# Kernel optimization log

Measured on AMD Instinct MI355X. Metric: run time of the kernel, lower is better.

The kernel has to match this reference:

```python
import jax, jax.numpy as jnp
import numpy as np

DT, TAU_S, TAU_M = 1.0, 4.0, 20.0
ALPHA = float(np.exp(-DT / TAU_S))   # synaptic current decay
BETA = float(np.exp(-DT / TAU_M))    # membrane potential decay
THRESH = 1.0
STEPS, BATCH, D1, D2 = 128, 256, 1024, 1024


def setup_inputs() -> dict:
    key = jax.random.key(0)
    k1, k2 = jax.random.split(key)
    inp = jax.random.uniform(k1, (STEPS, BATCH, D1), dtype=jnp.float32)
    # kaiming_normal_ on (d2, d1): std = sqrt(2 / fan_in), mu = 1.0
    weight = jax.random.normal(k2, (D2, D1), dtype=jnp.float32) * np.sqrt(2.0 / D1)
    return {"input": inp, "weight": weight}


def reference(input, weight):
    steps, batch = input.shape[0], input.shape[1]
    d2 = weight.shape[0]
    # Step i uses input[i-1]; precompute all linear projections at once.
    lin = jnp.einsum('tbi,oi->tbo', input[:-1], weight)  # [steps-1, B, d2]

    def step(carry, cur):
        syn, mem = carry
        # snntorch Synaptic, reset_mechanism='zero': reset from PREVIOUS mem
        reset = (mem > THRESH).astype(mem.dtype)
        syn = ALPHA * syn + cur
        mem = (BETA * mem + syn) * (1.0 - reset)
        spk = (mem > THRESH).astype(mem.dtype)
        return (syn, mem), (spk, mem, syn)

    init = (jnp.zeros((batch, d2), input.dtype), jnp.zeros((batch, d2), input.dtype))
    _, (spk, V, I) = jax.lax.scan(step, init, lin)
    z = jnp.zeros((1, batch, d2), input.dtype)  # step 0 stays zero
    output = jnp.concatenate([z, spk], axis=0)
    V = jnp.concatenate([z, V], axis=0)
    I = jnp.concatenate([z, I], axis=0)
    return output, V, I
```

## Files before the change

kernel.cpp:

```cpp
#include <hip/hip_runtime.h>
#include <hip/hip_fp16.h>


#define STEPS 128
#define BATCH 256
#define DIN   1024
#define DOUT  1024

#define ALPHA 0.7788007830714049f
#define BETA  0.9512294245007140f

constexpr int    GM      = (STEPS - 1) * BATCH;
constexpr size_t PLANE   = (size_t)BATCH * DOUT;
constexpr size_t A_ELEMS = (size_t)GM * DIN;
constexpr size_t W_ELEMS = (size_t)DOUT * DIN;

typedef __attribute__((ext_vector_type(8))) _Float16 half8;
typedef __attribute__((ext_vector_type(4))) float float4v;

__global__ __launch_bounds__(256)
void split_kernel(const float* __restrict__ x,
                  unsigned short* __restrict__ hi,
                  unsigned short* __restrict__ lo)
{
    const size_t i = (size_t)blockIdx.x * 256 + threadIdx.x;
    const float4 v = reinterpret_cast<const float4*>(x)[i];
    float f[4] = {v.x, v.y, v.z, v.w};
    unsigned short hb[4], lb[4];
#pragma unroll
    for (int j = 0; j < 4; ++j) {
        _Float16 h = (_Float16)f[j];
        _Float16 l = (_Float16)(f[j] - (float)h);
        hb[j] = *reinterpret_cast<unsigned short*>(&h);
        lb[j] = *reinterpret_cast<unsigned short*>(&l);
    }
    ushort4 hv = {hb[0], hb[1], hb[2], hb[3]};
    ushort4 lv = {lb[0], lb[1], lb[2], lb[3]};
    reinterpret_cast<ushort4*>(hi)[i] = hv;
    reinterpret_cast<ushort4*>(lo)[i] = lv;
}

__device__ __forceinline__ void load16(const unsigned short* g, unsigned short* l)
{
    __builtin_amdgcn_global_load_lds(
        (const __attribute__((address_space(1))) void*)g,
        (__attribute__((address_space(3))) void*)l, 16, 0, 0);
}

__device__ __forceinline__ half8 ldsr(unsigned addr)
{
    half8 r;
    asm volatile("ds_read_b128 %0, %1" : "=v"(r) : "v"(addr) : "memory");
    return r;
}

__global__ __launch_bounds__(512, 2)
void gemm_kernel(const unsigned short* __restrict__ Ah,
                 const unsigned short* __restrict__ Al,
                 const unsigned short* __restrict__ Wh,
                 const unsigned short* __restrict__ Wl,
                 float* __restrict__ C)
{
    __shared__ __align__(16) unsigned short smem[65536];

    const int lin = blockIdx.x;
    const int xcd = lin & 7, slot = lin >> 3;
    const int mp  = xcd * 16 + (slot >> 2);
    const int nt  = slot & 3;
    if (mp >= GM / 256) return;
    const int m0 = mp * 256;
    const int n0 = nt * 256;

    const int t = threadIdx.x;
    const int w = t >> 6, l = t & 63;
    const int wr = w >> 2, wc = w & 3;
    const int lr = l & 15, q = l >> 4;

    const int swz = q ^ ((l >> 1) & 3);

    const unsigned rdA = (unsigned)((wr * 128 + lr) * 64 + swz * 16);
    const unsigned rdB = (unsigned)(32768 + (wc * 64 + lr) * 64 + swz * 16);

    const int srow = l >> 2;
    const int sg   = ((l & 3) ^ ((l >> 3) & 3)) * 8;

    const size_t sA0 = (size_t)(m0 + w * 32 +      srow) * DIN + sg;
    const size_t sA1 = (size_t)(m0 + w * 32 + 16 + srow) * DIN + sg;
    const size_t sB0 = (size_t)(n0 + w * 32 +      srow) * DIN + sg;
    const size_t sB1 = (size_t)(n0 + w * 32 + 16 + srow) * DIN + sg;

    auto STAGE = [&](int ks) {
        const int kk = (ks & 31) << 5;
        unsigned short* d = smem + ((ks & 1) << 15) + w * 1024;
        load16(Ah + sA0 + kk, d);
        load16(Ah + sA1 + kk, d + 512);
        load16(Al + sA0 + kk, d + 8192);
        load16(Al + sA1 + kk, d + 8704);
        load16(Wh + sB0 + kk, d + 16384);
        load16(Wh + sB1 + kk, d + 16896);
        load16(Wl + sB0 + kk, d + 24576);
        load16(Wl + sB1 + kk, d + 25088);
    };

    float4v acc[8][4];
#pragma unroll
    for (int m = 0; m < 8; ++m)
#pragma unroll
        for (int n = 0; n < 4; ++n)
            acc[m][n] = (float4v){0.f, 0.f, 0.f, 0.f};

    STAGE(0);
    asm volatile("s_waitcnt vmcnt(0)" ::: "memory");
    __builtin_amdgcn_s_barrier();

    for (int kt = 0; kt < 32; ++kt) {
        const unsigned sb = (unsigned)((kt & 1) << 16);

        STAGE((kt + 1) & 31);

        half8 ah[8], bh[4], bl[4];

#pragma unroll
        for (int m = 0; m < 8; ++m) ah[m] = ldsr(sb + rdA + m * 1024);
#pragma unroll
        for (int n = 0; n < 4; ++n) bh[n] = ldsr(sb + rdB + n * 1024);
        asm volatile("s_waitcnt lgkmcnt(0)" ::: "memory");
        __builtin_amdgcn_sched_barrier(0);
        __builtin_amdgcn_s_setprio(1);
#pragma unroll
        for (int m = 0; m < 8; ++m)
#pragma unroll
            for (int n = 0; n < 4; ++n)
                acc[m][n] = __builtin_amdgcn_mfma_f32_16x16x32_f16(
                    ah[m], bh[n], acc[m][n], 0, 0, 0);
        __builtin_amdgcn_s_setprio(0);

#pragma unroll
        for (int n = 0; n < 4; ++n) bl[n] = ldsr(sb + rdB + 16384 + n * 1024);
        asm volatile("s_waitcnt lgkmcnt(0)" ::: "memory");
        __builtin_amdgcn_sched_barrier(0);
        __builtin_amdgcn_s_setprio(1);
#pragma unroll
        for (int m = 0; m < 8; ++m)
#pragma unroll
            for (int n = 0; n < 4; ++n)
                acc[m][n] = __builtin_amdgcn_mfma_f32_16x16x32_f16(
                    ah[m], bl[n], acc[m][n], 0, 0, 0);
        __builtin_amdgcn_s_setprio(0);

#pragma unroll
        for (int m = 0; m < 8; ++m) ah[m] = ldsr(sb + rdA + 16384 + m * 1024);
        asm volatile("s_waitcnt lgkmcnt(0)" ::: "memory");
        __builtin_amdgcn_sched_barrier(0);
        __builtin_amdgcn_s_setprio(1);
#pragma unroll
        for (int m = 0; m < 8; ++m)
#pragma unroll
            for (int n = 0; n < 4; ++n)
                acc[m][n] = __builtin_amdgcn_mfma_f32_16x16x32_f16(
                    ah[m], bh[n], acc[m][n], 0, 0, 0);
        __builtin_amdgcn_s_setprio(0);

        asm volatile("s_waitcnt vmcnt(0)" ::: "memory");
        __builtin_amdgcn_s_barrier();
    }

    const int mw = m0 + wr * 128 + q * 4;
    const int nw = n0 + wc * 64 + lr;
#pragma unroll
    for (int m = 0; m < 8; ++m)
#pragma unroll
        for (int n = 0; n < 4; ++n)
#pragma unroll
            for (int rg = 0; rg < 4; ++rg)
                C[(size_t)(mw + m * 16 + rg) * DOUT + (nw + n * 16)] = acc[m][n][rg];
}

__global__ __launch_bounds__(256)
void scan_kernel(float* __restrict__ out)
{
    const int idx = blockIdx.x * 256 + threadIdx.x;
    float* o0 = out;
    float* o1 = out + STEPS * PLANE;
    float* o2 = out + 2 * STEPS * PLANE;

    __builtin_nontemporal_store(0.0f, &o0[idx]);
    __builtin_nontemporal_store(0.0f, &o1[idx]);
    __builtin_nontemporal_store(0.0f, &o2[idx]);

    float n1 = o2[idx + PLANE];
    float n2 = o2[idx + 2 * PLANE];
    float n3 = o2[idx + 3 * PLANE];

    float syn = 0.0f, mem = 0.0f;
    size_t off = idx;
    for (int i = 1; i < STEPS; ++i) {
        off += PLANE;
        const float cur = n1; n1 = n2; n2 = n3;
        if (i + 3 < STEPS) n3 = o2[off + 3 * PLANE];
        const float reset = (mem > 1.0f) ? 1.0f : 0.0f;
        syn = ALPHA * syn + cur;
        mem = (BETA * mem + syn) * (1.0f - reset);
        const float spk = (mem > 1.0f) ? 1.0f : 0.0f;
        __builtin_nontemporal_store(spk, &o0[off]);
        __builtin_nontemporal_store(mem, &o1[off]);
        __builtin_nontemporal_store(syn, &o2[off]);
    }
}

extern "C" void kernel_launch(void* const* d_in, const int* in_sizes, int n_in,
                              void* d_out, int out_size, void* d_ws, size_t ws_size,
                              hipStream_t stream)
{
    const float* input  = (const float*)d_in[0];
    const float* weight = (const float*)d_in[1];
    float* out = (float*)d_out;

    unsigned short* Ah = (unsigned short*)out;
    unsigned short* Al = Ah + A_ELEMS;
    unsigned short* Wh = (unsigned short*)(out + STEPS * PLANE);
    unsigned short* Wl = Wh + W_ELEMS;
    float* lin = out + 2 * STEPS * PLANE + PLANE;

    split_kernel<<<(int)(A_ELEMS / 1024), 256, 0, stream>>>(input, Ah, Al);
    split_kernel<<<(int)(W_ELEMS / 1024), 256, 0, stream>>>(weight, Wh, Wl);

    gemm_kernel<<<512, 512, 0, stream>>>(Ah, Al, Wh, Wl, lin);

    scan_kernel<<<(int)(PLANE / 256), 256, 0, stream>>>(out);
}
```

Before: 686.5 us.

## Split GEMM k-loop into six barrier-synced phases with half-stage prefetch

The next k-tile's global-to-LDS staging is split into a hi half (A hi, W hi) and a lo half (A lo, W lo), each issued just before the phase that first needs it. A partial vmcnt(4) wait then lets the hi half of the next tile be consumed while the lo half is still in flight. Each of the three MFMA passes is split into two 4x4 sub-blocks, so only four A fragments are reloaded at a time, which lowers register pressure and interleaves LDS reads with matrix math. In exchange it adds many workgroup barriers per iteration, which may serialise the waves and hurt overlap between them.

```diff
diff --git a/kernel.cpp b/kernel.cpp
--- a/kernel.cpp
+++ b/kernel.cpp
@@ -54,6 +54,34 @@
     return r;
 }
 
+#define PHASE_PRE() do {                                        \
+    __builtin_amdgcn_s_barrier();                               \
+    asm volatile("s_waitcnt lgkmcnt(0)" ::: "memory");          \
+    __builtin_amdgcn_sched_barrier(0);                          \
+    __builtin_amdgcn_s_setprio(1);                              \
+} while (0)
+
+#define PHASE_POST() do {                                       \
+    __builtin_amdgcn_s_setprio(0);                              \
+    __builtin_amdgcn_sched_barrier(0);                          \
+    __builtin_amdgcn_s_barrier();                               \
+} while (0)
+
+#define PHASE_POST_VM4() do {                                   \
+    __builtin_amdgcn_s_setprio(0);                              \
+    __builtin_amdgcn_sched_barrier(0);                          \
+    asm volatile("s_waitcnt vmcnt(4)" ::: "memory");            \
+    __builtin_amdgcn_s_barrier();                               \
+} while (0)
+
+#define MFMA_BLK(MB, BV)                                        \
+    _Pragma("unroll")                                           \
+    for (int mm = 0; mm < 4; ++mm)                              \
+        _Pragma("unroll")                                       \
+        for (int nn = 0; nn < 4; ++nn)                          \
+            acc[(MB) + mm][nn] = __builtin_amdgcn_mfma_f32_16x16x32_f16( \
+                ah[(MB) + mm], BV[nn], acc[(MB) + mm][nn], 0, 0, 0)
+
 __global__ __launch_bounds__(512, 2)
 void gemm_kernel(const unsigned short* __restrict__ Ah,
                  const unsigned short* __restrict__ Al,
@@ -89,15 +117,19 @@
     const size_t sB0 = (size_t)(n0 + w * 32 +      srow) * DIN + sg;
     const size_t sB1 = (size_t)(n0 + w * 32 + 16 + srow) * DIN + sg;
 
-    auto STAGE = [&](int ks) {
+    auto STAGE_H1 = [&](int ks) {
         const int kk = (ks & 31) << 5;
         unsigned short* d = smem + ((ks & 1) << 15) + w * 1024;
         load16(Ah + sA0 + kk, d);
         load16(Ah + sA1 + kk, d + 512);
+        load16(Wh + sB0 + kk, d + 16384);
+        load16(Wh + sB1 + kk, d + 16896);
+    };
+    auto STAGE_H2 = [&](int ks) {
+        const int kk = (ks & 31) << 5;
+        unsigned short* d = smem + ((ks & 1) << 15) + w * 1024;
         load16(Al + sA0 + kk, d + 8192);
         load16(Al + sA1 + kk, d + 8704);
-        load16(Wh + sB0 + kk, d + 16384);
-        load16(Wh + sB1 + kk, d + 16896);
         load16(Wl + sB0 + kk, d + 24576);
         load16(Wl + sB1 + kk, d + 25088);
     };
@@ -109,60 +141,40 @@
         for (int n = 0; n < 4; ++n)
             acc[m][n] = (float4v){0.f, 0.f, 0.f, 0.f};
 
-    STAGE(0);
-    asm volatile("s_waitcnt vmcnt(0)" ::: "memory");
+    STAGE_H1(0);
+    STAGE_H2(0);
+    asm volatile("s_waitcnt vmcnt(4)" ::: "memory");
     __builtin_amdgcn_s_barrier();
 
     for (int kt = 0; kt < 32; ++kt) {
         const unsigned sb = (unsigned)((kt & 1) << 16);
-
-        STAGE((kt + 1) & 31);
-
         half8 ah[8], bh[4], bl[4];
 
 #pragma unroll
-        for (int m = 0; m < 8; ++m) ah[m] = ldsr(sb + rdA + m * 1024);
+        for (int m = 0; m < 4; ++m) ah[m] = ldsr(sb + rdA + m * 1024);
 #pragma unroll
         for (int n = 0; n < 4; ++n) bh[n] = ldsr(sb + rdB + n * 1024);
-        asm volatile("s_waitcnt lgkmcnt(0)" ::: "memory");
-        __builtin_amdgcn_sched_barrier(0);
-        __builtin_amdgcn_s_setprio(1);
-#pragma unroll
-        for (int m = 0; m < 8; ++m)
-#pragma unroll
-            for (int n = 0; n < 4; ++n)
-                acc[m][n] = __builtin_amdgcn_mfma_f32_16x16x32_f16(
-                    ah[m], bh[n], acc[m][n], 0, 0, 0);
-        __builtin_amdgcn_s_setprio(0);
+        STAGE_H1((kt + 1) & 31);
+        PHASE_PRE();  MFMA_BLK(0, bh);  PHASE_POST();
+
+#pragma unroll
+        for (int m = 4; m < 8; ++m) ah[m] = ldsr(sb + rdA + m * 1024);
+        PHASE_PRE();  MFMA_BLK(4, bh);  PHASE_POST_VM4();
 
 #pragma unroll
         for (int n = 0; n < 4; ++n) bl[n] = ldsr(sb + rdB + 16384 + n * 1024);
-        asm volatile("s_waitcnt lgkmcnt(0)" ::: "memory");
-        __builtin_amdgcn_sched_barrier(0);
-        __builtin_amdgcn_s_setprio(1);
-#pragma unroll
-        for (int m = 0; m < 8; ++m)
-#pragma unroll
-            for (int n = 0; n < 4; ++n)
-                acc[m][n] = __builtin_amdgcn_mfma_f32_16x16x32_f16(
-                    ah[m], bl[n], acc[m][n], 0, 0, 0);
-        __builtin_amdgcn_s_setprio(0);
-
-#pragma unroll
-        for (int m = 0; m < 8; ++m) ah[m] = ldsr(sb + rdA + 16384 + m * 1024);
-        asm volatile("s_waitcnt lgkmcnt(0)" ::: "memory");
-        __builtin_amdgcn_sched_barrier(0);
-        __builtin_amdgcn_s_setprio(1);
-#pragma unroll
-        for (int m = 0; m < 8; ++m)
-#pragma unroll
-            for (int n = 0; n < 4; ++n)
-                acc[m][n] = __builtin_amdgcn_mfma_f32_16x16x32_f16(
-                    ah[m], bh[n], acc[m][n], 0, 0, 0);
-        __builtin_amdgcn_s_setprio(0);
-
-        asm volatile("s_waitcnt vmcnt(0)" ::: "memory");
-        __builtin_amdgcn_s_barrier();
+        STAGE_H2((kt + 1) & 31);
+        PHASE_PRE();  MFMA_BLK(0, bl);  PHASE_POST();
+
+#pragma unroll
+        for (int m = 0; m < 4; ++m) ah[m] = ldsr(sb + rdA + 16384 + m * 1024);
+        PHASE_PRE();  MFMA_BLK(4, bl);  PHASE_POST();
+
+#pragma unroll
+        for (int m = 4; m < 8; ++m) ah[m] = ldsr(sb + rdA + 16384 + m * 1024);
+        PHASE_PRE();  MFMA_BLK(0, bh);  PHASE_POST();
+
+        PHASE_PRE();  MFMA_BLK(4, bh);  PHASE_POST_VM4();
     }
 
     const int mw = m0 + wr * 128 + q * 4;
```

Measured after the change: 682.9 us. Within noise of the previous version (-0.5%).
